# Kernel optimization log

Measured on AMD Instinct MI355X. Metric: run time of the kernel, lower is better.

Reference implementation:

```python
import jax, jax.numpy as jnp
import numpy as np
import math

V, T, D, H, L, B = 50257, 1024, 768, 12, 6, 2
FF = 4 * D
HD = D // H

def layernorm(x, g, b, eps=1e-5):
    mu = jnp.mean(x, axis=-1, keepdims=True)
    var = jnp.var(x, axis=-1, keepdims=True)
    return (x - mu) * jax.lax.rsqrt(var + eps) * g + b

def new_gelu(x):
    # Faithful to the (buggy) NewGelu: tanh arg = sqrt(2/pi) * 0.044715 * x**4
    c = math.sqrt(2.0 / math.pi)
    return 0.5 * x * (1.0 + jnp.tanh(c * (x * 0.044715 * jnp.power(x, 3))))

def setup_inputs() -> dict:
    key = jax.random.key(0)
    ks = jax.random.split(key, 18)
    n = lambda k, shape, s=0.02: (jax.random.normal(k, shape, dtype=jnp.float32) * s)
    return {
        "ids": jax.random.randint(ks[0], (B, T), 0, V),
        "wte": n(ks[1], (V, D)),
        "wpe": n(ks[2], (T, D)),
        "W_qkv": n(ks[3], (L, D, 3 * D)),
        "b_qkv": jnp.zeros((L, 3 * D), jnp.float32),
        "W_o": n(ks[4], (L, D, D)),
        "b_o": jnp.zeros((L, D), jnp.float32),
        "ln1_g": jnp.ones((L, D), jnp.float32),
        "ln1_b": jnp.zeros((L, D), jnp.float32),
        "W1": n(ks[5], (L, D, FF)),
        "b1": jnp.zeros((L, FF), jnp.float32),
        "W2": n(ks[6], (L, FF, D)),
        "b2": jnp.zeros((L, D), jnp.float32),
        "lnf_g": jnp.ones((D,), jnp.float32),
        "lnf_b": jnp.zeros((D,), jnp.float32),
        "W_head": n(ks[7], (D, V)),
        "b_head": jnp.zeros((V,), jnp.float32),
    }

def reference(ids, wte, wpe, W_qkv, b_qkv, W_o, b_o, ln1_g, ln1_b,
              W1, b1, W2, b2, lnf_g, lnf_b, W_head, b_head):
    t = ids.shape[1]
    x = wte[ids] + wpe[:t][None]  # [B,T,D]
    scale = 1.0 / math.sqrt(HD)
    for l in range(L):
        qkv = x @ W_qkv[l] + b_qkv[l]                 # [B,T,3D]
        q, k, v = jnp.split(qkv, 3, axis=-1)
        q = q.reshape(-1, t, H, HD).transpose(0, 2, 1, 3)  # [B,H,T,hd]
        k = k.reshape(-1, t, H, HD).transpose(0, 2, 1, 3)
        v = v.reshape(-1, t, H, HD).transpose(0, 2, 1, 3)
        # NOTE: mask buffer is all-ones in the source, so NO causal masking.
        att = jax.nn.softmax(jnp.einsum('bhqd,bhkd->bhqk', q, k) * scale, axis=-1)
        y = jnp.einsum('bhqk,bhkd->bhqd', att, v)
        y = y.transpose(0, 2, 1, 3).reshape(-1, t, D)
        y = y @ W_o[l] + b_o[l]
        x = layernorm(y, ln1_g[l], ln1_b[l]) + x      # ln1 AFTER attn, per source
        h = new_gelu(x @ W1[l] + b1[l]) @ W2[l] + b2[l]  # ln2 unused, per source
        x = h + x
    x = layernorm(x, lnf_g, lnf_b)
    logits = x @ W_head + b_head
    return logits
```

## Files before the change

kernel.cpp:

```cpp
#include <hip/hip_runtime.h>
#include <hip/hip_bf16.h>
#include <math.h>
#include <stdint.h>

#define NL 6
#define NB 2
#define ST 1024
#define ND 768
#define NH 12
#define HD 64
#define NFF 3072
#define NV 50257
#define ND3 2304
#define NM (NB * ST)

typedef short bf16x4 __attribute__((ext_vector_type(4)));
typedef short bf16x8 __attribute__((ext_vector_type(8)));
typedef float f32x4  __attribute__((ext_vector_type(4)));

typedef __attribute__((address_space(3))) void as3_void;
typedef __attribute__((address_space(1))) void as1_void;

__device__ __forceinline__ void async_copy16(const void* g, void* lds) {
  __builtin_amdgcn_global_load_lds((const as1_void*)(uintptr_t)g,
                                   (as3_void*)(uint32_t)(uintptr_t)lds,
                                   16, 0, 0);
}

__device__ __forceinline__ unsigned short f2bf(float f) {
  union { float f; uint32_t u; } v; v.f = f;
  return (unsigned short)((v.u + 0x7fffu + ((v.u >> 16) & 1u)) >> 16);
}

__device__ __forceinline__ bf16x8 frag16(const unsigned short* p) {
  return *(const bf16x8*)p;
}

template <int N>
__device__ __forceinline__ void wait_vm_barrier() {
  if constexpr (N == 8)      asm volatile("s_waitcnt vmcnt(8)\n\ts_barrier" ::: "memory");
  else if constexpr (N == 6) asm volatile("s_waitcnt vmcnt(6)\n\ts_barrier" ::: "memory");
  else if constexpr (N == 4) asm volatile("s_waitcnt vmcnt(4)\n\ts_barrier" ::: "memory");
  else                       asm volatile("s_waitcnt vmcnt(0)\n\ts_barrier" ::: "memory");
}
__device__ __forceinline__ void lgkm_barrier() {
  asm volatile("s_waitcnt lgkmcnt(0)\n\ts_barrier" ::: "memory");
}

#define MFMA(a, b, c) __builtin_amdgcn_mfma_f32_16x16x32_bf16((a), (b), (c), 0, 0, 0)

__device__ __forceinline__ float gelu_buggy(float x) {
  const float c = 0.7978845608028654f;
  float x2 = x * x;
  return 0.5f * x * (1.0f + tanhf(c * 0.044715f * x2 * x2));
}

enum { EP_QKV = 0, EP_PROJ, EP_FF1, EP_FF2, EP_HEAD };

template <int EPI, int TM, int TN, int WN, int NW, int BK, int NBUF>
__global__ __launch_bounds__(NW * 64)
void gemm_bt(const unsigned short* __restrict__ A,
             const unsigned short* __restrict__ BT,
             const float* __restrict__ bias,
             float* __restrict__ Cf,
             unsigned short* __restrict__ Cb,
             const float* __restrict__ resid,
             unsigned short* __restrict__ vT,
             int M, int N, int K)
{
  constexpr int WM = NW / WN;
  constexpr int FM = TM / WM / 16;
  constexpr int FN = TN / WN / 16;
  constexpr int SL = BK / 8;
  constexpr int RS = (BK == 32) ? 1 : 0;
  constexpr int RPC = 1024 / (BK * 2);
  constexpr int CA = TM / RPC / NW;
  constexpr int CB = TN / RPC / NW;
  constexpr int LPT = CA + CB;
  constexpr int KK = BK / 32;
  constexpr int DEPTH = NBUF - 1;
  __shared__ __align__(16) unsigned short As[NBUF][TM * BK];
  __shared__ __align__(16) unsigned short Bs[NBUF][TN * BK];
  const int tid = threadIdx.x;
  const int w = tid >> 6, l = tid & 63;
  const int g = l >> 4, r = l & 15;
  const int wm = (w / WN) * (FM * 16);
  const int wn = (w % WN) * (FN * 16);

  const int nbx = gridDim.x;
  const int nwg = nbx * gridDim.y;
  int bid = blockIdx.y * nbx + blockIdx.x;
  if ((nwg & 7) == 0) bid = (bid & 7) * (nwg >> 3) + (bid >> 3);
  const int m0 = (bid % nbx) * TM, n0 = (bid / nbx) * TN;

  const int sr = l / (BK / 8);
  const int se = ((l & (SL - 1)) ^ ((sr >> RS) & (SL - 1))) * 8;
  long aoff[CA];
  long boff[CB];
#pragma unroll
  for (int c = 0; c < CA; ++c) {
    const int arow = (w * CA + c) * RPC + sr;
    aoff[c] = (long)(m0 + arow) * K + se;
  }
#pragma unroll
  for (int c = 0; c < CB; ++c) {
    int brow = n0 + (w * CB + c) * RPC + sr;
    if (brow > N - 1) brow = N - 1;
    boff[c] = (long)brow * K + se;
  }

  f32x4 acc[FM][FN] = {};

  auto stage = [&](int t, int buf) {
    const long k0 = (long)t * BK;
#pragma unroll
    for (int c = 0; c < CA; ++c)
      async_copy16(A + aoff[c] + k0, &As[buf][(w * CA + c) * 512]);
#pragma unroll
    for (int c = 0; c < CB; ++c)
      async_copy16(BT + boff[c] + k0, &Bs[buf][(w * CB + c) * 512]);
  };

  auto compute = [&](int buf) {
#pragma unroll
    for (int kk = 0; kk < KK; ++kk) {
      bf16x8 af[FM], bf[FN];
#pragma unroll
      for (int mi = 0; mi < FM; ++mi)
        af[mi] = frag16(&As[buf][(wm + mi * 16 + r) * BK +
                                 (((kk * 4 + g) ^ ((r >> RS) & (SL - 1))) * 8)]);
#pragma unroll
      for (int ni = 0; ni < FN; ++ni)
        bf[ni] = frag16(&Bs[buf][(wn + ni * 16 + r) * BK +
                                 (((kk * 4 + g) ^ ((r >> RS) & (SL - 1))) * 8)]);
      __builtin_amdgcn_s_setprio(1);
#pragma unroll
      for (int mi = 0; mi < FM; ++mi)
#pragma unroll
        for (int ni = 0; ni < FN; ++ni)
          acc[mi][ni] = MFMA(af[mi], bf[ni], acc[mi][ni]);
      __builtin_amdgcn_s_setprio(0);
    }
  };

  const int nt = K / BK;
  stage(0, 0);
  if (DEPTH == 2) stage(1, 1);
  int cur = 0, nxt = DEPTH;
  for (int t = 0; t < nt; ++t) {
    const bool have_next = (t + DEPTH) < nt;
    if (have_next) stage(t + DEPTH, nxt);
    if (have_next && DEPTH == 2)       wait_vm_barrier<2 * LPT>();
    else if (have_next || (DEPTH == 2 && t + 1 < nt)) wait_vm_barrier<LPT>();
    else                               wait_vm_barrier<0>();
    compute(cur);
    if (t + 1 < nt) lgkm_barrier();
    cur = (cur + 1 == NBUF) ? 0 : cur + 1;
    nxt = (nxt + 1 == NBUF) ? 0 : nxt + 1;
  }

#pragma unroll
  for (int mi = 0; mi < FM; ++mi) {
#pragma unroll
    for (int ni = 0; ni < FN; ++ni) {
      const int col = n0 + wn + ni * 16 + r;
      if (EPI == EP_HEAD && col >= N) continue;
      const float bb = bias[col];
      if (EPI == EP_QKV && col >= 2 * ND) {
        const int hv = (col - 2 * ND) >> 6, d = (col - 2 * ND) & 63;
        short4 vv;
#pragma unroll
        for (int q = 0; q < 4; ++q)
          vv[q] = (short)f2bf(acc[mi][ni][q] + bb);
        const int row = m0 + wm + mi * 16 + g * 4;
        const int bb_ = row >> 10, t4 = row & 1023;
        *(short4*)&vT[(((long)bb_ * NH + hv) * HD + d) * ST + t4] = vv;
        continue;
      }
#pragma unroll
      for (int q = 0; q < 4; ++q) {
        const int row = m0 + wm + mi * 16 + g * 4 + q;
        float v = acc[mi][ni][q] + bb;
        if constexpr (EPI == EP_QKV) {
          Cb[(long)row * N + col] = f2bf(v);
        } else if constexpr (EPI == EP_PROJ) {
          Cf[(long)row * N + col] = v;
        } else if constexpr (EPI == EP_FF1) {
          Cb[(long)row * N + col] = f2bf(gelu_buggy(v));
        } else if constexpr (EPI == EP_FF2) {
          float o = v + resid[(long)row * N + col];
          Cf[(long)row * N + col] = o;
          Cb[(long)row * N + col] = f2bf(o);
        } else {
          Cf[(long)row * N + col] = v;
        }
      }
    }
  }
}

__global__ __launch_bounds__(256)
void attn_kernel(const unsigned short* __restrict__ qkv,
                 const unsigned short* __restrict__ vT,
                 unsigned short* __restrict__ y)
{
  constexpr int LS = 72;
  __shared__ __align__(16) unsigned short Qs[64 * LS];
  __shared__ __align__(16) unsigned short Ks[64 * LS];
  __shared__ __align__(16) unsigned short Vt[64 * LS];
  __shared__ __align__(16) unsigned short Ps[64 * LS];
  const int tid = threadIdx.x;
  const int w = tid >> 6, l = tid & 63;
  const int g = l >> 4, r = l & 15;
  const int q0 = blockIdx.x * 64;
  const int b = blockIdx.y / NH, h = blockIdx.y % NH;
  const long rb = (long)b * ST;
  const long vbase = ((long)b * NH + h) * HD * ST;
  const int srow = tid >> 3, sc8 = (tid & 7) * 8;

#pragma unroll
  for (int p = 0; p < 2; ++p) {
    const int row = p * 32 + srow;
    bf16x8 v = *(const bf16x8*)&qkv[(rb + q0 + row) * ND3 + h * HD + sc8];
    *(bf16x8*)&Qs[row * LS + sc8] = v;
  }
  __syncthreads();
  bf16x8 aq[2];
#pragma unroll
  for (int kk = 0; kk < 2; ++kk)
    aq[kk] = *(const bf16x8*)&Qs[(w * 16 + r) * LS + kk * 32 + g * 8];

  float m_run[4] = {-1e30f, -1e30f, -1e30f, -1e30f};
  float l_run[4] = {0.f, 0.f, 0.f, 0.f};
  f32x4 acc_o[4] = {};

  for (int kt = 0; kt < ST / 64; ++kt) {
#pragma unroll
    for (int p = 0; p < 2; ++p) {
      const int row = p * 32 + srow;
      *(bf16x8*)&Ks[row * LS + sc8] =
          *(const bf16x8*)&qkv[(rb + kt * 64 + row) * ND3 + ND + h * HD + sc8];
      *(bf16x8*)&Vt[row * LS + sc8] =
          *(const bf16x8*)&vT[vbase + (long)row * ST + kt * 64 + sc8];
    }
    __syncthreads();

    f32x4 s_acc[4] = {};
#pragma unroll
    for (int kk = 0; kk < 2; ++kk) {
#pragma unroll
      for (int ni = 0; ni < 4; ++ni) {
        bf16x8 bk = *(const bf16x8*)&Ks[(ni * 16 + r) * LS + kk * 32 + g * 8];
        s_acc[ni] = MFMA(aq[kk], bk, s_acc[ni]);
      }
    }

    float mloc[4];
#pragma unroll
    for (int q = 0; q < 4; ++q) {
      float mx = fmaxf(fmaxf(s_acc[0][q], s_acc[1][q]), fmaxf(s_acc[2][q], s_acc[3][q]));
      mloc[q] = mx * 0.125f;
    }
#pragma unroll
    for (int mask = 1; mask < 16; mask <<= 1)
#pragma unroll
      for (int q = 0; q < 4; ++q)
        mloc[q] = fmaxf(mloc[q], __shfl_xor(mloc[q], mask, 64));

    float alpha[4], psum[4] = {0.f, 0.f, 0.f, 0.f};
#pragma unroll
    for (int q = 0; q < 4; ++q) {
      const float mn = fmaxf(m_run[q], mloc[q]);
      alpha[q] = __expf(m_run[q] - mn);
      m_run[q] = mn;
    }
#pragma unroll
    for (int ni = 0; ni < 4; ++ni)
#pragma unroll
      for (int q = 0; q < 4; ++q) {
        const float p = __expf(s_acc[ni][q] * 0.125f - m_run[q]);
        psum[q] += p;
        Ps[(w * 16 + g * 4 + q) * LS + ni * 16 + r] = f2bf(p);
      }
#pragma unroll
    for (int mask = 1; mask < 16; mask <<= 1)
#pragma unroll
      for (int q = 0; q < 4; ++q) psum[q] += __shfl_xor(psum[q], mask, 64);
#pragma unroll
    for (int q = 0; q < 4; ++q) l_run[q] = l_run[q] * alpha[q] + psum[q];
#pragma unroll
    for (int ni = 0; ni < 4; ++ni)
#pragma unroll
      for (int q = 0; q < 4; ++q) acc_o[ni][q] *= alpha[q];

    asm volatile("s_waitcnt lgkmcnt(0)" ::: "memory");
    __builtin_amdgcn_sched_barrier(0);

#pragma unroll
    for (int kk = 0; kk < 2; ++kk) {
      bf16x8 ap = *(const bf16x8*)&Ps[(w * 16 + r) * LS + kk * 32 + g * 8];
#pragma unroll
      for (int ni = 0; ni < 4; ++ni) {
        bf16x8 bv = *(const bf16x8*)&Vt[(ni * 16 + r) * LS + kk * 32 + g * 8];
        acc_o[ni] = MFMA(ap, bv, acc_o[ni]);
      }
    }
    __syncthreads();
  }

#pragma unroll
  for (int ni = 0; ni < 4; ++ni)
#pragma unroll
    for (int q = 0; q < 4; ++q) {
      const int row = q0 + w * 16 + g * 4 + q;
      const int col = h * HD + ni * 16 + r;
      y[(rb + row) * ND + col] = f2bf(acc_o[ni][q] / l_run[q]);
    }
}

template <bool RESID>
__global__ __launch_bounds__(256)
void ln_kernel(const float* __restrict__ in, const float* __restrict__ resid,
               const float* __restrict__ gamma, const float* __restrict__ beta,
               float* __restrict__ out_f, unsigned short* __restrict__ out_b)
{
  __shared__ float wred[8];
  const int row = blockIdx.x, tid = threadIdx.x;
  float v[3];
#pragma unroll
  for (int j = 0; j < 3; ++j) v[j] = in[(long)row * ND + tid + j * 256];
  float s = v[0] + v[1] + v[2];
#pragma unroll
  for (int m = 1; m < 64; m <<= 1) s += __shfl_xor(s, m, 64);
  if ((tid & 63) == 0) wred[tid >> 6] = s;
  __syncthreads();
  const float mean = (wred[0] + wred[1] + wred[2] + wred[3]) * (1.0f / ND);
  float d[3];
#pragma unroll
  for (int j = 0; j < 3; ++j) d[j] = v[j] - mean;
  float s2 = d[0] * d[0] + d[1] * d[1] + d[2] * d[2];
#pragma unroll
  for (int m = 1; m < 64; m <<= 1) s2 += __shfl_xor(s2, m, 64);
  if ((tid & 63) == 0) wred[4 + (tid >> 6)] = s2;
  __syncthreads();
  const float var = (wred[4] + wred[5] + wred[6] + wred[7]) * (1.0f / ND);
  const float rstd = rsqrtf(var + 1e-5f);
#pragma unroll
  for (int j = 0; j < 3; ++j) {
    const int c = tid + j * 256;
    float o = d[j] * rstd * gamma[c] + beta[c];
    if (RESID) o += resid[(long)row * ND + c];
    if (out_f) out_f[(long)row * ND + c] = o;
    if (out_b) out_b[(long)row * ND + c] = f2bf(o);
  }
}

__global__ __launch_bounds__(256)
void embed_kernel(const int* __restrict__ ids, const float* __restrict__ wte,
                  const float* __restrict__ wpe, float* __restrict__ x,
                  unsigned short* __restrict__ xb)
{
  const int t = blockIdx.x, tid = threadIdx.x;
  const int tok = ids[t];
  const int pos = t & (ST - 1);
#pragma unroll
  for (int j = 0; j < 3; ++j) {
    const int c = tid + j * 256;
    const float v = wte[(long)tok * ND + c] + wpe[(long)pos * ND + c];
    x[(long)t * ND + c] = v;
    xb[(long)t * ND + c] = f2bf(v);
  }
}

__global__ __launch_bounds__(256)
void transpose_bf16(const float* __restrict__ in, unsigned short* __restrict__ out,
                    int R, int C)
{
  __shared__ float tile[64][33];
  const long z = (long)blockIdx.z * R * C;
  const int c0 = blockIdx.x * 32, r0 = blockIdx.y * 64;
  const int tx = threadIdx.x & 31, ty = threadIdx.x >> 5;
#pragma unroll
  for (int j = 0; j < 8; ++j) {
    const int rr = r0 + j * 8 + ty, cc = c0 + tx;
    if (cc < C) tile[j * 8 + ty][tx] = in[z + (long)rr * C + cc];
  }
  __syncthreads();
  const int rx = threadIdx.x & 63, cy = threadIdx.x >> 6;
#pragma unroll
  for (int j = 0; j < 8; ++j) {
    const int cc = c0 + j * 4 + cy;
    if (cc < C) out[z + (long)cc * R + r0 + rx] = f2bf(tile[rx][j * 4 + cy]);
  }
}

extern "C" void kernel_launch(void* const* d_in, const int* in_sizes, int n_in,
                              void* d_out, int out_size, void* d_ws, size_t ws_size,
                              hipStream_t stream)
{
  const int*   ids    = (const int*)d_in[0];
  const float* wte    = (const float*)d_in[1];
  const float* wpe    = (const float*)d_in[2];
  const float* W_qkv  = (const float*)d_in[3];
  const float* b_qkv  = (const float*)d_in[4];
  const float* W_o    = (const float*)d_in[5];
  const float* b_o    = (const float*)d_in[6];
  const float* ln1_g  = (const float*)d_in[7];
  const float* ln1_b  = (const float*)d_in[8];
  const float* W1     = (const float*)d_in[9];
  const float* b1     = (const float*)d_in[10];
  const float* W2     = (const float*)d_in[11];
  const float* b2     = (const float*)d_in[12];
  const float* lnf_g  = (const float*)d_in[13];
  const float* lnf_b  = (const float*)d_in[14];
  const float* W_head = (const float*)d_in[15];
  const float* b_head = (const float*)d_in[16];
  float* out = (float*)d_out;
  (void)in_sizes; (void)n_in; (void)out_size; (void)ws_size;

  char* ws = (char*)d_ws;
  size_t off = 0;
  auto alloc = [&](size_t bytes) -> void* {
    void* p = (void*)(ws + off);
    off = (off + bytes + 255) & ~(size_t)255;
    return p;
  };
  unsigned short* wqkvT = (unsigned short*)alloc((size_t)NL * ND3 * ND * 2);
  unsigned short* woT   = (unsigned short*)alloc((size_t)NL * ND * ND * 2);
  unsigned short* w1T   = (unsigned short*)alloc((size_t)NL * NFF * ND * 2);
  unsigned short* w2T   = (unsigned short*)alloc((size_t)NL * ND * NFF * 2);
  unsigned short* whT   = (unsigned short*)alloc((size_t)NV * ND * 2);
  float*          xf    = (float*)alloc((size_t)NM * ND * 4);
  unsigned short* xb    = (unsigned short*)alloc((size_t)NM * ND * 2);
  unsigned short* qkvb  = (unsigned short*)alloc((size_t)NM * ND3 * 2);
  unsigned short* yb    = (unsigned short*)alloc((size_t)NM * ND * 2);
  float*          aof   = (float*)alloc((size_t)NM * ND * 4);
  unsigned short* h1b   = (unsigned short*)alloc((size_t)NM * NFF * 2);
  unsigned short* xlnb  = (unsigned short*)alloc((size_t)NM * ND * 2);
  unsigned short* vtb   = (unsigned short*)alloc((size_t)NB * NH * HD * ST * 2);

  dim3 tb(256);
  dim3 tb128(128);
  dim3 tb512(512);
  transpose_bf16<<<dim3(ND3 / 32, ND / 64, NL), tb, 0, stream>>>(W_qkv, wqkvT, ND, ND3);
  transpose_bf16<<<dim3(ND / 32, ND / 64, NL), tb, 0, stream>>>(W_o, woT, ND, ND);
  transpose_bf16<<<dim3(NFF / 32, ND / 64, NL), tb, 0, stream>>>(W1, w1T, ND, NFF);
  transpose_bf16<<<dim3(ND / 32, NFF / 64, NL), tb, 0, stream>>>(W2, w2T, NFF, ND);
  transpose_bf16<<<dim3((NV + 31) / 32, ND / 64, 1), tb, 0, stream>>>(W_head, whT, ND, NV);

  embed_kernel<<<dim3(NM), tb, 0, stream>>>(ids, wte, wpe, xf, xb);

  for (int l = 0; l < NL; ++l) {
    gemm_bt<EP_QKV, 128, 64, 2, 4, 64, 2><<<dim3(NM / 128, ND3 / 64), tb, 0, stream>>>(
        xb, wqkvT + (size_t)l * ND3 * ND, b_qkv + (size_t)l * ND3,
        nullptr, qkvb, nullptr, vtb, NM, ND3, ND);
    attn_kernel<<<dim3(ST / 64, NB * NH), tb, 0, stream>>>(qkvb, vtb, yb);
    gemm_bt<EP_PROJ, 64, 64, 2, 2, 64, 2><<<dim3(NM / 64, ND / 64), tb128, 0, stream>>>(
        yb, woT + (size_t)l * ND * ND, b_o + (size_t)l * ND,
        aof, nullptr, nullptr, nullptr, NM, ND, ND);
    ln_kernel<true><<<dim3(NM), tb, 0, stream>>>(
        aof, xf, ln1_g + (size_t)l * ND, ln1_b + (size_t)l * ND, xf, xb);
    gemm_bt<EP_FF1, 128, 64, 2, 4, 64, 2><<<dim3(NM / 128, NFF / 64), tb, 0, stream>>>(
        xb, w1T + (size_t)l * NFF * ND, b1 + (size_t)l * NFF,
        nullptr, h1b, nullptr, nullptr, NM, NFF, ND);
    gemm_bt<EP_FF2, 64, 64, 2, 2, 64, 2><<<dim3(NM / 64, ND / 64), tb128, 0, stream>>>(
        h1b, w2T + (size_t)l * ND * NFF, b2 + (size_t)l * ND,
        xf, xb, xf, nullptr, NM, ND, NFF);
  }
  ln_kernel<false><<<dim3(NM), tb, 0, stream>>>(xf, nullptr, lnf_g, lnf_b, nullptr, xlnb);
  gemm_bt<EP_HEAD, 256, 256, 4, 8, 32, 3><<<dim3(NM / 256, (NV + 255) / 256), tb512, 0, stream>>>(
      xlnb, whT, b_head, out, nullptr, nullptr, nullptr, NM, NV, ND);
}
```

Before: 1.132 ms.

## Use wave-per-row layernorm, add occupancy hints, retile LM-head GEMM

Layernorm now has each 64-lane wave handle one row with 12 values per lane, so the block-wide LDS reduction and both __syncthreads are gone, and each block covers four rows. The GEMM kernel gains a min-blocks-per-CU launch bound to push the compiler toward fewer registers and more resident blocks. The LM-head GEMM moves to a 128-row tile with double buffering instead of 256 rows with triple buffering, which lowers LDS and register use and doubles the grid. New vmcnt wait variants are added to support the new pipeline depth. The tighter register budget could cause spills in the larger GEMM configurations.

After: 1.160 ms. 2.5% more time.

```diff
diff --git a/kernel.cpp b/kernel.cpp
--- a/kernel.cpp
+++ b/kernel.cpp
@@ -40,7 +40,10 @@
 __device__ __forceinline__ void wait_vm_barrier() {
   if constexpr (N == 8)      asm volatile("s_waitcnt vmcnt(8)\n\ts_barrier" ::: "memory");
   else if constexpr (N == 6) asm volatile("s_waitcnt vmcnt(6)\n\ts_barrier" ::: "memory");
+  else if constexpr (N == 5) asm volatile("s_waitcnt vmcnt(5)\n\ts_barrier" ::: "memory");
   else if constexpr (N == 4) asm volatile("s_waitcnt vmcnt(4)\n\ts_barrier" ::: "memory");
+  else if constexpr (N == 3) asm volatile("s_waitcnt vmcnt(3)\n\ts_barrier" ::: "memory");
+  else if constexpr (N == 2) asm volatile("s_waitcnt vmcnt(2)\n\ts_barrier" ::: "memory");
   else                       asm volatile("s_waitcnt vmcnt(0)\n\ts_barrier" ::: "memory");
 }
 __device__ __forceinline__ void lgkm_barrier() {
@@ -58,7 +61,7 @@
 enum { EP_QKV = 0, EP_PROJ, EP_FF1, EP_FF2, EP_HEAD };
 
 template <int EPI, int TM, int TN, int WN, int NW, int BK, int NBUF>
-__global__ __launch_bounds__(NW * 64)
+__global__ __launch_bounds__(NW * 64, NW == 8 ? 4 : 2)
 void gemm_bt(const unsigned short* __restrict__ A,
              const unsigned short* __restrict__ BT,
              const float* __restrict__ bias,
@@ -324,31 +327,28 @@
                const float* __restrict__ gamma, const float* __restrict__ beta,
                float* __restrict__ out_f, unsigned short* __restrict__ out_b)
 {
-  __shared__ float wred[8];
-  const int row = blockIdx.x, tid = threadIdx.x;
-  float v[3];
-#pragma unroll
-  for (int j = 0; j < 3; ++j) v[j] = in[(long)row * ND + tid + j * 256];
-  float s = v[0] + v[1] + v[2];
+  const int w = threadIdx.x >> 6, l = threadIdx.x & 63;
+  const int row = blockIdx.x * 4 + w;
+  const float* p = in + (long)row * ND;
+  float v[12];
+#pragma unroll
+  for (int j = 0; j < 12; ++j) v[j] = p[l + j * 64];
+  float s = 0.f;
+#pragma unroll
+  for (int j = 0; j < 12; ++j) s += v[j];
 #pragma unroll
   for (int m = 1; m < 64; m <<= 1) s += __shfl_xor(s, m, 64);
-  if ((tid & 63) == 0) wred[tid >> 6] = s;
-  __syncthreads();
-  const float mean = (wred[0] + wred[1] + wred[2] + wred[3]) * (1.0f / ND);
-  float d[3];
-#pragma unroll
-  for (int j = 0; j < 3; ++j) d[j] = v[j] - mean;
-  float s2 = d[0] * d[0] + d[1] * d[1] + d[2] * d[2];
+  const float mean = s * (1.0f / ND);
+  float s2 = 0.f;
+#pragma unroll
+  for (int j = 0; j < 12; ++j) { v[j] -= mean; s2 += v[j] * v[j]; }
 #pragma unroll
   for (int m = 1; m < 64; m <<= 1) s2 += __shfl_xor(s2, m, 64);
-  if ((tid & 63) == 0) wred[4 + (tid >> 6)] = s2;
-  __syncthreads();
-  const float var = (wred[4] + wred[5] + wred[6] + wred[7]) * (1.0f / ND);
-  const float rstd = rsqrtf(var + 1e-5f);
-#pragma unroll
-  for (int j = 0; j < 3; ++j) {
-    const int c = tid + j * 256;
-    float o = d[j] * rstd * gamma[c] + beta[c];
+  const float rstd = rsqrtf(s2 * (1.0f / ND) + 1e-5f);
+#pragma unroll
+  for (int j = 0; j < 12; ++j) {
+    const int c = l + j * 64;
+    float o = v[j] * rstd * gamma[c] + beta[c];
     if (RESID) o += resid[(long)row * ND + c];
     if (out_f) out_f[(long)row * ND + c] = o;
     if (out_b) out_b[(long)row * ND + c] = f2bf(o);
@@ -458,7 +458,7 @@
     gemm_bt<EP_PROJ, 64, 64, 2, 2, 64, 2><<<dim3(NM / 64, ND / 64), tb128, 0, stream>>>(
         yb, woT + (size_t)l * ND * ND, b_o + (size_t)l * ND,
         aof, nullptr, nullptr, nullptr, NM, ND, ND);
-    ln_kernel<true><<<dim3(NM), tb, 0, stream>>>(
+    ln_kernel<true><<<dim3(NM / 4), tb, 0, stream>>>(
         aof, xf, ln1_g + (size_t)l * ND, ln1_b + (size_t)l * ND, xf, xb);
     gemm_bt<EP_FF1, 128, 64, 2, 4, 64, 2><<<dim3(NM / 128, NFF / 64), tb, 0, stream>>>(
         xb, w1T + (size_t)l * NFF * ND, b1 + (size_t)l * NFF,
@@ -467,7 +467,7 @@
         h1b, w2T + (size_t)l * ND * NFF, b2 + (size_t)l * ND,
         xf, xb, xf, nullptr, NM, ND, NFF);
   }
-  ln_kernel<false><<<dim3(NM), tb, 0, stream>>>(xf, nullptr, lnf_g, lnf_b, nullptr, xlnb);
-  gemm_bt<EP_HEAD, 256, 256, 4, 8, 32, 3><<<dim3(NM / 256, (NV + 255) / 256), tb512, 0, stream>>>(
+  ln_kernel<false><<<dim3(NM / 4), tb, 0, stream>>>(xf, nullptr, lnf_g, lnf_b, nullptr, xlnb);
+  gemm_bt<EP_HEAD, 128, 256, 4, 8, 32, 2><<<dim3(NM / 128, (NV + 255) / 256), tb512, 0, stream>>>(
       xlnb, whT, b_head, out, nullptr, nullptr, nullptr, NM, NV, ND);
 }
```
